# Kernel optimization log

Measured on AMD Instinct MI355X. Metric: run time of the kernel, lower is better.

## Reference

```python
import math
import jax, jax.numpy as jnp
import numpy as np

FACIL_RATE = 2.0
FIRE_THRESH = 0.85
MAX_GATE = 8.0
EPS = 1e-12  # F.normalize eps

B, T, D = 8, 4096, 2048


def _gelu(x):
    # tanh-approx GELU, exactly as in the torch module
    c = math.sqrt(2.0 / math.pi)
    return 0.5 * x * (1.0 + jnp.tanh(c * (x + 0.044715 * x * x * x)))


def _l2norm(v, axis=-1):
    n = jnp.sqrt(jnp.sum(v * v, axis=axis, keepdims=True))
    return v / jnp.maximum(n, EPS)


def setup_inputs() -> dict:
    key = jax.random.key(0)
    k1, k2 = jax.random.split(key)
    x = jax.random.normal(k1, (B, T, D), dtype=jnp.float32)
    pos_buf = jax.random.normal(k2, (T, D), dtype=jnp.float32)
    pos_facil = jnp.ones((T,), dtype=jnp.float32)
    log_k_pos = jnp.asarray(math.log(0.5), dtype=jnp.float32)
    return {"x": x, "log_k_pos": log_k_pos, "pos_buf": pos_buf, "pos_facil": pos_facil}


def reference(x, log_k_pos, pos_buf, pos_facil):
    # steady-state (pass1 complete) path of GELU275.forward
    k_pos = jnp.clip(jnp.exp(log_k_pos), 0.01, 5.0)
    y = _gelu(x)                                   # [B,T,D]
    # everything below the gelu except the final gate multiply runs under
    # no_grad / on y.detach() in torch -> stop_gradient here
    y_det = jax.lax.stop_gradient(y)
    pos_buf_n = _l2norm(jax.lax.stop_gradient(pos_buf))          # [T,D]
    y_n = _l2norm(y_det)                                          # [B,T,D]
    sim = jnp.einsum("btd,td->bt", y_n, pos_buf_n)               # cosine sim [B,T]
    fire_mask = jnp.mean(sim, axis=0) > FIRE_THRESH              # [T]
    pf = jax.lax.stop_gradient(pos_facil)
    facil_t = jnp.where(fire_mask, jnp.minimum(pf * FACIL_RATE, 16.0), pf)  # [T]
    gate = jnp.minimum(1.0 + k_pos * (facil_t[None, :] - 1.0) * sim, MAX_GATE)  # [B,T]
    return y * gate[:, :, None]
```

## Files before the change

### kernel.cpp

```cpp
#include <hip/hip_runtime.h>
#include <math.h>

#define BB 8
#define TT 4096
#define DD 2048
#define THREADS 512
#define NT 4
#define NBLK (TT / NT)

typedef float v4f __attribute__((ext_vector_type(4)));

__device__ __forceinline__ float gelu_fast(float x) {
    const float c1 = 1.5957691216057308f;
    const float c2 = 0.07135481282556483f;
    float e = __expf(-x * fmaf(c2, x * x, c1));
    return x * __builtin_amdgcn_rcpf(1.0f + e);
}

__device__ __forceinline__ void do_step(
    const float* __restrict__ xp,
    const float* __restrict__ pp,
    const float* __restrict__ pos_facil, float* __restrict__ op,
    int t, int par, bool last, int lane, int wave, float kp,
    v4f (&CUR)[8], v4f (&NXT)[8],
    float (&s_red)[2][17])
{
    if (!last) {
#pragma unroll
        for (int c = 0; c < 8; ++c)
            NXT[c] = *(const v4f*)(xp + DD + c * 256);
    }

    float dot = 0.f, yn2 = 0.f, pn2 = 0.f;
#pragma unroll
    for (int c = 0; c < 8; ++c) {
        const v4f p = *(const v4f*)(pp + c * 256);
        v4f v = CUR[c];
        v.x = gelu_fast(v.x); v.y = gelu_fast(v.y);
        v.z = gelu_fast(v.z); v.w = gelu_fast(v.w);
        CUR[c] = v;
        dot += v.x * p.x + v.y * p.y + v.z * p.z + v.w * p.w;
        yn2 += v.x * v.x + v.y * v.y + v.z * v.z + v.w * v.w;
        pn2 += p.x * p.x + p.y * p.y + p.z * p.z + p.w * p.w;
    }

#pragma unroll
    for (int off = 32; off; off >>= 1) {
        dot += __shfl_xor(dot, off);
        yn2 += __shfl_xor(yn2, off);
        pn2 += __shfl_xor(pn2, off);
    }
    if (lane == 0) {
        s_red[par][wave]      = dot;
        s_red[par][BB + wave] = yn2;
        if (wave == 0) s_red[par][16] = pn2;
    }
    asm volatile("s_waitcnt lgkmcnt(0)" ::: "memory");
    __builtin_amdgcn_s_barrier();
    asm volatile("" ::: "memory");

    const float pnn = fmaxf(sqrtf(s_red[par][16]), 1e-12f);
    float simsum = 0.f, simw = 0.f;
#pragma unroll
    for (int b = 0; b < BB; ++b) {
        const float s = s_red[par][b] *
            __builtin_amdgcn_rcpf(fmaxf(sqrtf(s_red[par][BB + b]), 1e-12f) * pnn);
        simsum += s;
        if (b == wave) simw = s;
    }
    const bool  fire  = (simsum * 0.125f) > 0.85f;
    const float pf    = pos_facil[t];
    const float facil = fire ? fminf(pf * 2.0f, 16.0f) : pf;
    const float g     = fminf(1.0f + kp * (facil - 1.0f) * simw, 8.0f);

#pragma unroll
    for (int c = 0; c < 8; ++c) {
        v4f o = CUR[c];
        o.x *= g; o.y *= g; o.z *= g; o.w *= g;
        *(v4f*)(op + c * 256) = o;
    }
}

__global__ __launch_bounds__(THREADS, 6) void gelu275_fused(
    const float* __restrict__ x,
    const float* __restrict__ log_k_pos,
    const float* __restrict__ pos_buf,
    const float* __restrict__ pos_facil,
    float* __restrict__ out)
{
    const int tid  = threadIdx.x;
    const int lane = tid & 63;
    const int wave = tid >> 6;
    const int t0   = blockIdx.x * NT;

    __shared__ float s_red[2][17];

    const float kp   = fminf(fmaxf(__expf(log_k_pos[0]), 0.01f), 5.0f);
    const int   base = lane * 4;

    const float* xp = x       + ((size_t)wave * TT + t0) * DD + base;
    const float* pp = pos_buf + (size_t)t0 * DD + base;
    float*       op = out     + ((size_t)wave * TT + t0) * DD + base;

    v4f A[8], B[8];

#pragma unroll
    for (int c = 0; c < 8; ++c) A[c] = *(const v4f*)(xp + c * 256);

#pragma unroll
    for (int i = 0; i < NT; i += 2) {
        do_step(xp, pp, pos_facil, op, t0 + i, 0, false,
                lane, wave, kp, A, B, s_red);
        xp += DD; pp += DD; op += DD;
        do_step(xp, pp, pos_facil, op, t0 + i + 1, 1, (i + 2 >= NT),
                lane, wave, kp, B, A, s_red);
        xp += DD; pp += DD; op += DD;
    }
}

extern "C" void kernel_launch(void* const* d_in, const int* in_sizes, int n_in,
                              void* d_out, int out_size, void* d_ws, size_t ws_size,
                              hipStream_t stream) {
    const float* x          = (const float*)d_in[0];
    const float* log_k_pos  = (const float*)d_in[1];
    const float* pos_buf    = (const float*)d_in[2];
    const float* pos_facil  = (const float*)d_in[3];
    float* out              = (float*)d_out;

    dim3 grid(NBLK);
    dim3 block(THREADS);
    gelu275_fused<<<grid, block, 0, stream>>>(x, log_k_pos, pos_buf, pos_facil, out);
}
```

Measured before the change: 143.7 us.

## Split each row across two waves and deepen prefetch to two rows ahead

Doubles the block to 1024 threads so each batch row's 2048-wide vector is split across two waves, each holding 4 v4f per row instead of 8. The x loads now use a 3-slot ring buffer that prefetches two timesteps ahead, and pos_buf is prefetched one step ahead. Each block handles 8 timesteps, with a cross-half reduction through shared memory. The aim is more memory-level parallelism and lower register pressure per wave, at the cost of larger blocks, more barrier participants and fewer blocks in the grid.

New measurement: 130.7 us. 1.1x faster.

```diff
diff --git a/kernel.cpp b/kernel.cpp
--- a/kernel.cpp
+++ b/kernel.cpp
@@ -4,8 +4,8 @@
 #define BB 8
 #define TT 4096
 #define DD 2048
-#define THREADS 512
-#define NT 4
+#define THREADS 1024
+#define NT 8
 #define NBLK (TT / NT)
 
 typedef float v4f __attribute__((ext_vector_type(4)));
@@ -17,71 +17,7 @@
     return x * __builtin_amdgcn_rcpf(1.0f + e);
 }
 
-__device__ __forceinline__ void do_step(
-    const float* __restrict__ xp,
-    const float* __restrict__ pp,
-    const float* __restrict__ pos_facil, float* __restrict__ op,
-    int t, int par, bool last, int lane, int wave, float kp,
-    v4f (&CUR)[8], v4f (&NXT)[8],
-    float (&s_red)[2][17])
-{
-    if (!last) {
-#pragma unroll
-        for (int c = 0; c < 8; ++c)
-            NXT[c] = *(const v4f*)(xp + DD + c * 256);
-    }
-
-    float dot = 0.f, yn2 = 0.f, pn2 = 0.f;
-#pragma unroll
-    for (int c = 0; c < 8; ++c) {
-        const v4f p = *(const v4f*)(pp + c * 256);
-        v4f v = CUR[c];
-        v.x = gelu_fast(v.x); v.y = gelu_fast(v.y);
-        v.z = gelu_fast(v.z); v.w = gelu_fast(v.w);
-        CUR[c] = v;
-        dot += v.x * p.x + v.y * p.y + v.z * p.z + v.w * p.w;
-        yn2 += v.x * v.x + v.y * v.y + v.z * v.z + v.w * v.w;
-        pn2 += p.x * p.x + p.y * p.y + p.z * p.z + p.w * p.w;
-    }
-
-#pragma unroll
-    for (int off = 32; off; off >>= 1) {
-        dot += __shfl_xor(dot, off);
-        yn2 += __shfl_xor(yn2, off);
-        pn2 += __shfl_xor(pn2, off);
-    }
-    if (lane == 0) {
-        s_red[par][wave]      = dot;
-        s_red[par][BB + wave] = yn2;
-        if (wave == 0) s_red[par][16] = pn2;
-    }
-    asm volatile("s_waitcnt lgkmcnt(0)" ::: "memory");
-    __builtin_amdgcn_s_barrier();
-    asm volatile("" ::: "memory");
-
-    const float pnn = fmaxf(sqrtf(s_red[par][16]), 1e-12f);
-    float simsum = 0.f, simw = 0.f;
-#pragma unroll
-    for (int b = 0; b < BB; ++b) {
-        const float s = s_red[par][b] *
-            __builtin_amdgcn_rcpf(fmaxf(sqrtf(s_red[par][BB + b]), 1e-12f) * pnn);
-        simsum += s;
-        if (b == wave) simw = s;
-    }
-    const bool  fire  = (simsum * 0.125f) > 0.85f;
-    const float pf    = pos_facil[t];
-    const float facil = fire ? fminf(pf * 2.0f, 16.0f) : pf;
-    const float g     = fminf(1.0f + kp * (facil - 1.0f) * simw, 8.0f);
-
-#pragma unroll
-    for (int c = 0; c < 8; ++c) {
-        v4f o = CUR[c];
-        o.x *= g; o.y *= g; o.z *= g; o.w *= g;
-        *(v4f*)(op + c * 256) = o;
-    }
-}
-
-__global__ __launch_bounds__(THREADS, 6) void gelu275_fused(
+__global__ __launch_bounds__(THREADS, 4) void gelu275_fused(
     const float* __restrict__ x,
     const float* __restrict__ log_k_pos,
     const float* __restrict__ pos_buf,
@@ -91,30 +27,98 @@
     const int tid  = threadIdx.x;
     const int lane = tid & 63;
     const int wave = tid >> 6;
+    const int b    = wave & 7;
+    const int h    = wave >> 3;
     const int t0   = blockIdx.x * NT;
 
-    __shared__ float s_red[2][17];
+    __shared__ float s_red[2][48];
 
     const float kp   = fminf(fmaxf(__expf(log_k_pos[0]), 0.01f), 5.0f);
-    const int   base = lane * 4;
+    const int   base = h * 1024 + lane * 4;
 
-    const float* xp = x       + ((size_t)wave * TT + t0) * DD + base;
+    const float* xp = x       + ((size_t)b * TT + t0) * DD + base;
     const float* pp = pos_buf + (size_t)t0 * DD + base;
-    float*       op = out     + ((size_t)wave * TT + t0) * DD + base;
+    float*       op = out     + ((size_t)b * TT + t0) * DD + base;
 
-    v4f A[8], B[8];
+    v4f X[3][4];
+    v4f P[4];
 
 #pragma unroll
-    for (int c = 0; c < 8; ++c) A[c] = *(const v4f*)(xp + c * 256);
+    for (int c = 0; c < 4; ++c) X[0][c] = *(const v4f*)(xp + c * 256);
+#pragma unroll
+    for (int c = 0; c < 4; ++c) X[1][c] = *(const v4f*)(xp + DD + c * 256);
+#pragma unroll
+    for (int c = 0; c < 4; ++c) P[c]    = *(const v4f*)(pp + c * 256);
 
 #pragma unroll
-    for (int i = 0; i < NT; i += 2) {
-        do_step(xp, pp, pos_facil, op, t0 + i, 0, false,
-                lane, wave, kp, A, B, s_red);
-        xp += DD; pp += DD; op += DD;
-        do_step(xp, pp, pos_facil, op, t0 + i + 1, 1, (i + 2 >= NT),
-                lane, wave, kp, B, A, s_red);
-        xp += DD; pp += DD; op += DD;
+    for (int i = 0; i < NT; ++i) {
+        const int cur = i % 3;
+        const int nxt = (i + 2) % 3;
+        const int par = i & 1;
+
+        if (i + 2 < NT) {
+#pragma unroll
+            for (int c = 0; c < 4; ++c)
+                X[nxt][c] = *(const v4f*)(xp + (size_t)(i + 2) * DD + c * 256);
+        }
+
+        float dot = 0.f, yn2 = 0.f, pn2 = 0.f;
+#pragma unroll
+        for (int c = 0; c < 4; ++c) {
+            v4f v = X[cur][c];
+            const v4f p = P[c];
+            v.x = gelu_fast(v.x); v.y = gelu_fast(v.y);
+            v.z = gelu_fast(v.z); v.w = gelu_fast(v.w);
+            X[cur][c] = v;
+            dot += v.x * p.x + v.y * p.y + v.z * p.z + v.w * p.w;
+            yn2 += v.x * v.x + v.y * v.y + v.z * v.z + v.w * v.w;
+            pn2 += p.x * p.x + p.y * p.y + p.z * p.z + p.w * p.w;
+        }
+
+        if (i + 1 < NT) {
+#pragma unroll
+            for (int c = 0; c < 4; ++c)
+                P[c] = *(const v4f*)(pp + (size_t)(i + 1) * DD + c * 256);
+        }
+
+#pragma unroll
+        for (int off = 32; off; off >>= 1) {
+            dot += __shfl_xor(dot, off);
+            yn2 += __shfl_xor(yn2, off);
+            pn2 += __shfl_xor(pn2, off);
+        }
+        if (lane == 0) {
+            s_red[par][wave]      = dot;
+            s_red[par][16 + wave] = yn2;
+            s_red[par][32 + wave] = pn2;
+        }
+        asm volatile("s_waitcnt lgkmcnt(0)" ::: "memory");
+        __builtin_amdgcn_s_barrier();
+        asm volatile("" ::: "memory");
+
+        const float pn2t = s_red[par][32] + s_red[par][40];
+        const float pnn  = fmaxf(sqrtf(pn2t), 1e-12f);
+        float simsum = 0.f, simb = 0.f;
+#pragma unroll
+        for (int bb = 0; bb < BB; ++bb) {
+            const float dt = s_red[par][bb]      + s_red[par][8 + bb];
+            const float yt = s_red[par][16 + bb] + s_red[par][24 + bb];
+            const float s  = dt *
+                __builtin_amdgcn_rcpf(fmaxf(sqrtf(yt), 1e-12f) * pnn);
+            simsum += s;
+            if (bb == b) simb = s;
+        }
+        const bool  fire  = (simsum * 0.125f) > 0.85f;
+        const float pf    = pos_facil[t0 + i];
+        const float facil = fire ? fminf(pf * 2.0f, 16.0f) : pf;
+        const float g     = fminf(1.0f + kp * (facil - 1.0f) * simb, 8.0f);
+
+#pragma unroll
+        for (int c = 0; c < 4; ++c) {
+            v4f o = X[cur][c];
+            o.x *= g; o.y *= g; o.z *= g; o.w *= g;
+            *(v4f*)(op + (size_t)i * DD + c * 256) = o;
+        }
     }
 }
 
```
